# Optimization experiments

Measured on AMD Instinct MI355X. Metric: run time of the kernel, lower is better.

## Reference

```python
import jax, jax.numpy as jnp
import numpy as np

N, E, M, C = 4000, 60000, 16, 64        # nodes, edges, (lmax+1)^2, sphere_channels
H, HEADS, A, VC, CE, Z = 64, 8, 8, 8, 32, 90  # attn hidden, heads, alpha ch, value ch, edge ch, max elements


def _params(key):
    ks = jax.random.split(key, 10)
    g = lambda k, sh, fan: jax.random.normal(k, sh, dtype=jnp.float32) / np.float32(np.sqrt(fan))
    return [g(ks[0], (Z, CE), CE),          # emb_s: source atom embedding
            g(ks[1], (Z, CE), CE),          # emb_t: target atom embedding
            g(ks[2], (CE,), 1.0),           # w_d : distance projection
            g(ks[3], (CE, H), CE),          # We  : edge scalar -> hidden (m=0 inject)
            g(ks[4], (C, H), C),            # Ws  : source channel mix
            g(ks[5], (C, H), C),            # Wt  : target channel mix
            g(ks[6], (H, HEADS * A), H),    # Wa  : alpha features
            g(ks[7], (HEADS, A), A),        # va  : per-head alpha vector
            g(ks[8], (H, HEADS * VC), H),   # Wv  : values
            g(ks[9], (HEADS * VC, 1), HEADS * VC)]  # Wo : output proj (1 channel)


def setup_inputs() -> dict:
    key = jax.random.key(0)
    ks = jax.random.split(key, 8)
    x = jax.random.normal(ks[0], (N, M, C), dtype=jnp.float32)
    atomic_numbers = jax.random.randint(ks[1], (N,), 0, Z)
    edge_distance = jax.random.uniform(ks[2], (E,), dtype=jnp.float32) * 5.0 + 0.5
    edge_index = jax.random.randint(ks[3], (2, E), 0, N)
    noise_mask = jax.random.randint(ks[4], (N,), 0, 2).astype(bool)
    # per-edge SO3/Wigner rotation: random orthogonal [E, M, M]
    rng = np.random.default_rng(0)
    q, _ = np.linalg.qr(rng.standard_normal((E, M, M)).astype(np.float32))
    wigner = jnp.asarray(q, dtype=jnp.float32)
    names = ['emb_s', 'emb_t', 'w_d', 'We', 'Ws', 'Wt', 'Wa', 'va', 'Wv', 'Wo']
    inp = {'x': x, 'atomic_numbers': atomic_numbers, 'edge_distance': edge_distance,
           'edge_index': edge_index, 'noise_mask': noise_mask, 'wigner': wigner}
    for n, v in zip(names, _params(ks[5])):
        inp['fs_' + n] = v
    for n, v in zip(names, _params(ks[6])):
        inp['dn_' + n] = v
    return inp


def _block(x, zn, dist, src, dst, D, emb_s, emb_t, w_d, We, Ws, Wt, Wa, va, Wv, Wo):
    # gather + rotate edge-wise node features into edge-aligned frame
    xs = jnp.einsum('emn,enc->emc', D, x[src])            # [E,M,C]
    xt = jnp.einsum('emn,enc->emc', D, x[dst])            # [E,M,C]
    # scalar edge embedding (distance + source/target atom embeddings)
    e = jax.nn.silu(dist[:, None] * w_d + emb_s[zn[src]] + emb_t[zn[dst]])  # [E,CE]
    # SO2-style channel mixing; inject edge scalars into the m=0 (invariant) row
    f = jnp.einsum('emc,ch->emh', xs, Ws) + jnp.einsum('emc,ch->emh', xt, Wt)  # [E,M,H]
    f = f.at[:, 0, :].add(e @ We)
    # attention logits from the invariant part
    a = jax.nn.leaky_relu(f[:, 0, :] @ Wa, 0.2).reshape(E, HEADS, A)
    logits = jnp.einsum('eha,ha->eh', a, va)              # [E,HEADS]
    # segment softmax over incoming edges per target node
    mx = jax.ops.segment_max(logits, dst, num_segments=N)
    ex = jnp.exp(logits - mx[dst])
    alpha = ex / (jax.ops.segment_sum(ex, dst, num_segments=N)[dst] + 1e-9)
    # values, attention-weight, rotate back (D^T), scatter to nodes
    v = (f @ Wv).reshape(E, M, HEADS, VC) * alpha[:, None, :, None]
    v = jnp.einsum('emn,emhv->enhv', D, v).reshape(E, M, HEADS * VC)
    out = jax.ops.segment_sum(v, dst, num_segments=N) @ Wo  # [N,M,1]
    return out[:, 1:4, 0]  # narrow(1, 1, 3) -> l=1 vector components [N,3]


def reference(x, atomic_numbers, edge_distance, edge_index, noise_mask, wigner,
              fs_emb_s, fs_emb_t, fs_w_d, fs_We, fs_Ws, fs_Wt, fs_Wa, fs_va, fs_Wv, fs_Wo,
              dn_emb_s, dn_emb_t, dn_w_d, dn_We, dn_Ws, dn_Wt, dn_Wa, dn_va, dn_Wv, dn_Wo):
    src, dst = edge_index[0], edge_index[1]
    forces = _block(x, atomic_numbers, edge_distance, src, dst, wigner,
                    fs_emb_s, fs_emb_t, fs_w_d, fs_We, fs_Ws, fs_Wt, fs_Wa, fs_va, fs_Wv, fs_Wo)
    den = _block(x, atomic_numbers, edge_distance, src, dst, wigner,
                 dn_emb_s, dn_emb_t, dn_w_d, dn_We, dn_Ws, dn_Wt, dn_Wa, dn_va, dn_Wv, dn_Wo)
    # denoising_pos_forward with noise_mask: forces = den*mask + forces*~mask
    m = noise_mask[:, None].astype(x.dtype)
    return den * m + forces * (1.0 - m)
```

## Files before the change

kernel.cpp:

```cpp
#include <hip/hip_runtime.h>

typedef unsigned short ushort_t;
typedef __attribute__((ext_vector_type(8))) short short8;
typedef __attribute__((ext_vector_type(4))) float floatx4;

constexpr int RS = 11520;

__device__ inline float bf2f(ushort_t u) {
    union { unsigned int i; float f; } v; v.i = ((unsigned int)u) << 16; return v.f;
}
__device__ inline ushort_t f2bf(float f) {
    union { float f; unsigned int i; } v; v.f = f;
    unsigned int b = v.i + 0x7FFFu + ((v.i >> 16) & 1u);
    return (ushort_t)(b >> 16);
}

__global__ __launch_bounds__(256) void k_composites(
    const float* __restrict__ Ws0, const float* __restrict__ Wt0, const float* __restrict__ We0,
    const float* __restrict__ Wa0, const float* __restrict__ Wv0, const float* __restrict__ Wo0,
    const float* __restrict__ Ws1, const float* __restrict__ Wt1, const float* __restrict__ We1,
    const float* __restrict__ Wa1, const float* __restrict__ Wv1, const float* __restrict__ Wo1,
    float* __restrict__ cmp)
{
    int task = blockIdx.x;
    int r    = blockIdx.y;
    const float* Ws = r ? Ws1 : Ws0;
    const float* Wt = r ? Wt1 : Wt0;
    const float* We = r ? We1 : We0;
    const float* Wa = r ? Wa1 : Wa0;
    const float* Wv = r ? Wv1 : Wv0;
    const float* Wo = r ? Wo1 : Wo0;
    float* base = cmp + r * RS;

    if (task == 0 || task == 1) {
        const float* L = task ? Wt : Ws;
        float* out = base + task * 4096;
        for (int idx = threadIdx.x; idx < 4096; idx += 256) {
            int c = idx >> 6, j = idx & 63;
            float a = 0.f;
            for (int k = 0; k < 64; ++k) a += L[c * 64 + k] * Wa[k * 64 + j];
            out[idx] = a;
        }
    } else if (task == 2) {
        float* out = base + 8192;
        for (int idx = threadIdx.x; idx < 2048; idx += 256) {
            int ce = idx >> 6, j = idx & 63;
            float a = 0.f;
            for (int k = 0; k < 64; ++k) a += We[ce * 64 + k] * Wa[k * 64 + j];
            out[idx] = a;
        }
    } else {
        const float* L = (task == 3) ? Ws : (task == 4) ? Wt : We;
        int rows = (task == 5) ? 32 : 64;
        float* out = base + ((task == 3) ? 10240 : (task == 4) ? 10752 : 11264);
        for (int idx = threadIdx.x; idx < rows * 8; idx += 256) {
            int c = idx >> 3, h = idx & 7;
            float a = 0.f;
            for (int k = 0; k < 64; ++k) {
                float wv = 0.f;
                #pragma unroll
                for (int aa = 0; aa < 8; ++aa) wv += Wv[k * 64 + h * 8 + aa] * Wo[h * 8 + aa];
                a += L[c * 64 + k] * wv;
            }
            out[idx] = a;
        }
    }
}

__device__ inline short8 bfragW(const float* __restrict__ W, int colBase, int kBase,
                                int q, int n) {
    short8 f;
    #pragma unroll
    for (int j = 0; j < 8; ++j)
        f[j] = (short)f2bf(W[(kBase + q * 8 + j) * 64 + colBase + n]);
    return f;
}
__device__ inline short8 bfragP(const float* __restrict__ P0, const float* __restrict__ P1,
                                int kBase, int q, int n) {
    const float* P = (n < 8) ? P0 : P1;
    int c = n & 7;
    short8 f;
    #pragma unroll
    for (int j = 0; j < 8; ++j)
        f[j] = (short)f2bf(P[(kBase + q * 8 + j) * 8 + c]);
    return f;
}
__device__ inline void st4(ushort_t* dst, const floatx4& c) {
    uint2 v;
    v.x = (unsigned int)f2bf(c[0]) | ((unsigned int)f2bf(c[1]) << 16);
    v.y = (unsigned int)f2bf(c[2]) | ((unsigned int)f2bf(c[3]) << 16);
    *(uint2*)dst = v;
}

#define MFMA(a, b, c) __builtin_amdgcn_mfma_f32_16x16x32_bf16((a), (b), (c), 0, 0, 0)

__global__ __launch_bounds__(256, 2) void k_node(
    const float* __restrict__ x, const int* __restrict__ mask,
    const float* __restrict__ cmp,
    float* __restrict__ psrc, float* __restrict__ ptgt,
    ushort_t* __restrict__ srcA, ushort_t* __restrict__ tgtA,
    int N, int totWaves)
{
    int wid  = (int)((blockIdx.x * blockDim.x + threadIdx.x) >> 6);
    int lane = threadIdx.x & 63;
    int q    = lane >> 4;
    int n16  = lane & 15;

    short8 Bs0[4][2], Bs1[4][2], Bt0[4][2], Bt1[4][2];
    #pragma unroll
    for (int t = 0; t < 4; ++t) {
        #pragma unroll
        for (int kh = 0; kh < 2; ++kh) {
            Bs0[t][kh] = bfragW(cmp,             t * 16, kh * 32, q, n16);
            Bs1[t][kh] = bfragW(cmp + RS,        t * 16, kh * 32, q, n16);
            Bt0[t][kh] = bfragW(cmp + 4096,      t * 16, kh * 32, q, n16);
            Bt1[t][kh] = bfragW(cmp + RS + 4096, t * 16, kh * 32, q, n16);
        }
    }
    short8 Bp[2], Bq[2];
    #pragma unroll
    for (int kh = 0; kh < 2; ++kh) {
        Bp[kh] = bfragP(cmp + 10240, cmp + RS + 10240, kh * 32, q, n16);
        Bq[kh] = bfragP(cmp + 10752, cmp + RS + 10752, kh * 32, q, n16);
    }

    const floatx4 zero = {0.f, 0.f, 0.f, 0.f};

    for (int nd = wid; nd < N; nd += totWaves) {
        const float* xp = x + (size_t)nd * 1024 + n16 * 64 + q * 8;
        float4 v0 = *(const float4*)(xp);
        float4 v1 = *(const float4*)(xp + 4);
        float4 v2 = *(const float4*)(xp + 32);
        float4 v3 = *(const float4*)(xp + 36);
        short8 a0, a1;
        a0[0] = (short)f2bf(v0.x); a0[1] = (short)f2bf(v0.y);
        a0[2] = (short)f2bf(v0.z); a0[3] = (short)f2bf(v0.w);
        a0[4] = (short)f2bf(v1.x); a0[5] = (short)f2bf(v1.y);
        a0[6] = (short)f2bf(v1.z); a0[7] = (short)f2bf(v1.w);
        a1[0] = (short)f2bf(v2.x); a1[1] = (short)f2bf(v2.y);
        a1[2] = (short)f2bf(v2.z); a1[3] = (short)f2bf(v2.w);
        a1[4] = (short)f2bf(v3.x); a1[5] = (short)f2bf(v3.y);
        a1[6] = (short)f2bf(v3.z); a1[7] = (short)f2bf(v3.w);

        int rsel = (mask[nd] != 0);

        {
            floatx4 c0 = zero, c1 = zero, c2 = zero, c3 = zero;
            c0 = MFMA(a0, Bs0[0][0], c0); c0 = MFMA(a1, Bs0[0][1], c0);
            c1 = MFMA(a0, Bs0[1][0], c1); c1 = MFMA(a1, Bs0[1][1], c1);
            c2 = MFMA(a0, Bs0[2][0], c2); c2 = MFMA(a1, Bs0[2][1], c2);
            c3 = MFMA(a0, Bs0[3][0], c3); c3 = MFMA(a1, Bs0[3][1], c3);
            ushort_t* sp = srcA + (size_t)nd * 2048 + n16 * 16 + q * 4;
            st4(sp, c0); st4(sp + 256, c1); st4(sp + 512, c2); st4(sp + 768, c3);
        }
        {
            floatx4 c0 = zero, c1 = zero, c2 = zero, c3 = zero;
            c0 = MFMA(a0, Bs1[0][0], c0); c0 = MFMA(a1, Bs1[0][1], c0);
            c1 = MFMA(a0, Bs1[1][0], c1); c1 = MFMA(a1, Bs1[1][1], c1);
            c2 = MFMA(a0, Bs1[2][0], c2); c2 = MFMA(a1, Bs1[2][1], c2);
            c3 = MFMA(a0, Bs1[3][0], c3); c3 = MFMA(a1, Bs1[3][1], c3);
            ushort_t* sp = srcA + (size_t)nd * 2048 + 1024 + n16 * 16 + q * 4;
            st4(sp, c0); st4(sp + 256, c1); st4(sp + 512, c2); st4(sp + 768, c3);
        }

        {
            floatx4 c0 = zero, c1 = zero, c2 = zero, c3 = zero;
            if (rsel) {
                c0 = MFMA(a0, Bt1[0][0], c0); c0 = MFMA(a1, Bt1[0][1], c0);
                c1 = MFMA(a0, Bt1[1][0], c1); c1 = MFMA(a1, Bt1[1][1], c1);
                c2 = MFMA(a0, Bt1[2][0], c2); c2 = MFMA(a1, Bt1[2][1], c2);
                c3 = MFMA(a0, Bt1[3][0], c3); c3 = MFMA(a1, Bt1[3][1], c3);
            } else {
                c0 = MFMA(a0, Bt0[0][0], c0); c0 = MFMA(a1, Bt0[0][1], c0);
                c1 = MFMA(a0, Bt0[1][0], c1); c1 = MFMA(a1, Bt0[1][1], c1);
                c2 = MFMA(a0, Bt0[2][0], c2); c2 = MFMA(a1, Bt0[2][1], c2);
                c3 = MFMA(a0, Bt0[3][0], c3); c3 = MFMA(a1, Bt0[3][1], c3);
            }
            ushort_t* tp = tgtA + (size_t)nd * 1024 + n16 * 16 + q * 4;
            st4(tp, c0); st4(tp + 256, c1); st4(tp + 512, c2); st4(tp + 768, c3);
        }

        {
            floatx4 cp = zero;
            cp = MFMA(a0, Bp[0], cp); cp = MFMA(a1, Bp[1], cp);
            if (q == 0) {
                int r = n16 >> 3, h = n16 & 7;
                float* pp = psrc + (size_t)nd * 48 + r * 24 + h;
                pp[0]  = cp[1];
                pp[8]  = cp[2];
                pp[16] = cp[3];
            }
            floatx4 cq = zero;
            cq = MFMA(a0, Bq[0], cq); cq = MFMA(a1, Bq[1], cq);
            if (q == 0 && (n16 >> 3) == rsel) {
                int h = n16 & 7;
                float* pp = ptgt + (size_t)nd * 24 + h;
                pp[0]  = cq[1];
                pp[8]  = cq[2];
                pp[16] = cq[3];
            }
        }
    }
}

__global__ __launch_bounds__(256) void k_fused(
    const int* __restrict__ ei, const float* __restrict__ dist,
    const int* __restrict__ zn, const int* __restrict__ mask,
    const float* __restrict__ wig, const float* __restrict__ cmp,
    const float* __restrict__ embs0, const float* __restrict__ embt0, const float* __restrict__ wd0,
    const float* __restrict__ embs1, const float* __restrict__ embt1, const float* __restrict__ wd1,
    const float* __restrict__ va0, const float* __restrict__ va1,
    const ushort_t* __restrict__ srcA, const ushort_t* __restrict__ tgtA,
    const float* __restrict__ psrc, const float* __restrict__ ptgt,
    float* __restrict__ den, float* __restrict__ num, int E)
{
    int wv = threadIdx.x >> 6, j = threadIdx.x & 63;
    int e = blockIdx.x * 4 + wv;
    if (e >= E) return;
    int src = ei[e], dst = ei[E + e];
    int r = (mask[dst] != 0);
    float d = dist[e];
    int zs = zn[src], zt = zn[dst];
    int hq = j >> 3, h8 = j & 7;

    const float* w0 = wig + (size_t)e * 256;
    float4 wA = *(const float4*)(w0);
    float4 wB = *(const float4*)(w0 + 4);
    float4 wC = *(const float4*)(w0 + 8);
    float4 wD = *(const float4*)(w0 + 12);
    const ushort_t* sa = srcA + (size_t)src * 2048 + r * 1024 + j * 16;
    const ushort_t* ta = tgtA + (size_t)dst * 1024 + j * 16;
    short8 sv0 = *(const short8*)(sa);
    short8 sv1 = *(const short8*)(sa + 8);
    short8 tv0 = *(const short8*)(ta);
    short8 tv1 = *(const short8*)(ta + 8);
    float pv = 0.f;
    if (h8 < 3)
        pv = psrc[(size_t)src * 48 + r * 24 + h8 * 8 + hq]
           + ptgt[(size_t)dst * 24 + h8 * 8 + hq];

    float es;
    {
        int ce = j & 31;
        float z = r ? (d * wd1[ce] + embs1[zs * 32 + ce] + embt1[zt * 32 + ce])
                    : (d * wd0[ce] + embs0[zs * 32 + ce] + embt0[zt * 32 + ce]);
        es = z / (1.f + __expf(-z));
    }

    const float* WeWa   = cmp + r * RS + 8192;
    const float* WeWvWo = cmp + r * RS + 11264;
    float f0a = 0.f, ej = 0.f;
    #pragma unroll
    for (int ce = 0; ce < 32; ++ce) {
        float ev = __shfl(es, ce, 64);
        f0a += ev * WeWa[ce * 64 + j];
        ej  += ev * WeWvWo[ce * 8 + hq];
    }

    f0a += wA.x * (bf2f((ushort_t)sv0[0]) + bf2f((ushort_t)tv0[0]));
    f0a += wA.y * (bf2f((ushort_t)sv0[1]) + bf2f((ushort_t)tv0[1]));
    f0a += wA.z * (bf2f((ushort_t)sv0[2]) + bf2f((ushort_t)tv0[2]));
    f0a += wA.w * (bf2f((ushort_t)sv0[3]) + bf2f((ushort_t)tv0[3]));
    f0a += wB.x * (bf2f((ushort_t)sv0[4]) + bf2f((ushort_t)tv0[4]));
    f0a += wB.y * (bf2f((ushort_t)sv0[5]) + bf2f((ushort_t)tv0[5]));
    f0a += wB.z * (bf2f((ushort_t)sv0[6]) + bf2f((ushort_t)tv0[6]));
    f0a += wB.w * (bf2f((ushort_t)sv0[7]) + bf2f((ushort_t)tv0[7]));
    f0a += wC.x * (bf2f((ushort_t)sv1[0]) + bf2f((ushort_t)tv1[0]));
    f0a += wC.y * (bf2f((ushort_t)sv1[1]) + bf2f((ushort_t)tv1[1]));
    f0a += wC.z * (bf2f((ushort_t)sv1[2]) + bf2f((ushort_t)tv1[2]));
    f0a += wC.w * (bf2f((ushort_t)sv1[3]) + bf2f((ushort_t)tv1[3]));
    f0a += wD.x * (bf2f((ushort_t)sv1[4]) + bf2f((ushort_t)tv1[4]));
    f0a += wD.y * (bf2f((ushort_t)sv1[5]) + bf2f((ushort_t)tv1[5]));
    f0a += wD.z * (bf2f((ushort_t)sv1[6]) + bf2f((ushort_t)tv1[6]));
    f0a += wD.w * (bf2f((ushort_t)sv1[7]) + bf2f((ushort_t)tv1[7]));

    float la = f0a > 0.f ? f0a : 0.2f * f0a;
    float val = la * (r ? va1[j] : va0[j]);
    val += __shfl_xor(val, 1);
    val += __shfl_xor(val, 2);
    val += __shfl_xor(val, 4);
    float ex = __expf(val);

    if (h8 == 0) atomicAdd(&den[dst * 8 + hq], ex);
    if (h8 < 3) {
        float w0k = (h8 == 0) ? wA.y : (h8 == 1) ? wA.z : wA.w;
        atomicAdd(&num[dst * 24 + hq * 3 + h8], ex * (pv + ej * w0k));
    }
}

__global__ __launch_bounds__(256) void k_out(
    const float* __restrict__ num, const float* __restrict__ den,
    float* __restrict__ out, int N3)
{
    int t = blockIdx.x * 256 + threadIdx.x;
    if (t >= N3) return;
    int n = t / 3, k = t - n * 3;
    float acc = 0.f;
    #pragma unroll
    for (int h = 0; h < 8; ++h)
        acc += num[n * 24 + h * 3 + k] / (den[n * 8 + h] + 1e-9f);
    out[t] = acc;
}

extern "C" void kernel_launch(void* const* d_in, const int* in_sizes, int n_in,
                              void* d_out, int out_size, void* d_ws, size_t ws_size,
                              hipStream_t stream) {
    const float* x    = (const float*)d_in[0];
    const int*   zn   = (const int*)d_in[1];
    const float* dist = (const float*)d_in[2];
    const int*   ei   = (const int*)d_in[3];
    const int*   mask = (const int*)d_in[4];
    const float* wig  = (const float*)d_in[5];
    const float* fs[10]; const float* dn[10];
    for (int i = 0; i < 10; ++i) { fs[i] = (const float*)d_in[6 + i]; dn[i] = (const float*)d_in[16 + i]; }

    int N = in_sizes[1];
    int E = in_sizes[2];

    float* cmp  = (float*)d_ws;
    float* den  = cmp + 2 * RS;
    float* num  = den + (size_t)N * 8;
    float* psrc = num + (size_t)N * 24;
    float* ptgt = psrc + (size_t)N * 48;
    ushort_t* srcA = (ushort_t*)(ptgt + (size_t)N * 24);
    ushort_t* tgtA = srcA + (size_t)N * 2048;

    hipMemsetAsync(d_out, 0, (size_t)out_size * sizeof(float), stream);
    hipMemsetAsync(den, 0, (size_t)N * 32 * sizeof(float), stream);

    k_composites<<<dim3(6, 2), 256, 0, stream>>>(
        fs[4], fs[5], fs[3], fs[6], fs[8], fs[9],
        dn[4], dn[5], dn[3], dn[6], dn[8], dn[9], cmp);

    int nodeBlocks = 1000;
    int totWaves = nodeBlocks * (256 / 64);
    k_node<<<nodeBlocks, 256, 0, stream>>>(x, mask, cmp, psrc, ptgt, srcA, tgtA, N, totWaves);

    k_fused<<<(E + 3) / 4, 256, 0, stream>>>(
        ei, dist, zn, mask, wig, cmp,
        fs[0], fs[1], fs[2], dn[0], dn[1], dn[2],
        fs[7], dn[7], srcA, tgtA, psrc, ptgt, den, num, E);

    k_out<<<(N * 3 + 255) / 256, 256, 0, stream>>>(num, den, (float*)d_out, N * 3);
}
```

Before: 244.1 us.

## Prepack bf16 MFMA weight fragments, split composite kernel, process two edges per wave

The composite-weight kernel gains a z grid dimension that splits the Ws/Wt·Wa products across more blocks, and it writes those results directly as bf16 MFMA B-fragments into a packed buffer. k_node then loads each fragment with one short8 vector load instead of eight strided fp32 loads plus conversions per fragment in every wave. The fused edge kernel now handles two edges per wave, giving more independent loads in flight and halving the block count, at the cost of higher register pressure.

After: 246.5 us. Within noise of the previous version (+1.0%).

```diff
diff --git a/kernel.cpp b/kernel.cpp
--- a/kernel.cpp
+++ b/kernel.cpp
@@ -20,10 +20,11 @@
     const float* __restrict__ Wa0, const float* __restrict__ Wv0, const float* __restrict__ Wo0,
     const float* __restrict__ Ws1, const float* __restrict__ Wt1, const float* __restrict__ We1,
     const float* __restrict__ Wa1, const float* __restrict__ Wv1, const float* __restrict__ Wo1,
-    float* __restrict__ cmp)
+    float* __restrict__ cmp, ushort_t* __restrict__ packW)
 {
     int task = blockIdx.x;
     int r    = blockIdx.y;
+    int z    = blockIdx.z;
     const float* Ws = r ? Ws1 : Ws0;
     const float* Wt = r ? Wt1 : Wt0;
     const float* We = r ? We1 : We0;
@@ -34,22 +35,28 @@
 
     if (task == 0 || task == 1) {
         const float* L = task ? Wt : Ws;
-        float* out = base + task * 4096;
-        for (int idx = threadIdx.x; idx < 4096; idx += 256) {
-            int c = idx >> 6, j = idx & 63;
+        ushort_t* pw = packW + (r * 2 + task) * 4096;
+        int lo = z * 1024;
+        for (int idx = lo + threadIdx.x; idx < lo + 1024; idx += 256) {
+            int c = idx >> 6, jc = idx & 63;
             float a = 0.f;
-            for (int k = 0; k < 64; ++k) a += L[c * 64 + k] * Wa[k * 64 + j];
-            out[idx] = a;
+            #pragma unroll 8
+            for (int k = 0; k < 64; ++k) a += L[c * 64 + k] * Wa[k * 64 + jc];
+            int t = jc >> 4, n = jc & 15, kh = c >> 5, q = (c >> 3) & 3, jj = c & 7;
+            pw[((t * 2 + kh) * 64 + q * 16 + n) * 8 + jj] = f2bf(a);
         }
     } else if (task == 2) {
         float* out = base + 8192;
-        for (int idx = threadIdx.x; idx < 2048; idx += 256) {
-            int ce = idx >> 6, j = idx & 63;
+        int lo = z * 512;
+        for (int idx = lo + threadIdx.x; idx < lo + 512; idx += 256) {
+            int ce = idx >> 6, jc = idx & 63;
             float a = 0.f;
-            for (int k = 0; k < 64; ++k) a += We[ce * 64 + k] * Wa[k * 64 + j];
+            #pragma unroll 8
+            for (int k = 0; k < 64; ++k) a += We[ce * 64 + k] * Wa[k * 64 + jc];
             out[idx] = a;
         }
     } else {
+        if (z != 0) return;
         const float* L = (task == 3) ? Ws : (task == 4) ? Wt : We;
         int rows = (task == 5) ? 32 : 64;
         float* out = base + ((task == 3) ? 10240 : (task == 4) ? 10752 : 11264);
@@ -67,14 +74,6 @@
     }
 }
 
-__device__ inline short8 bfragW(const float* __restrict__ W, int colBase, int kBase,
-                                int q, int n) {
-    short8 f;
-    #pragma unroll
-    for (int j = 0; j < 8; ++j)
-        f[j] = (short)f2bf(W[(kBase + q * 8 + j) * 64 + colBase + n]);
-    return f;
-}
 __device__ inline short8 bfragP(const float* __restrict__ P0, const float* __restrict__ P1,
                                 int kBase, int q, int n) {
     const float* P = (n < 8) ? P0 : P1;
@@ -96,7 +95,7 @@
 
 __global__ __launch_bounds__(256, 2) void k_node(
     const float* __restrict__ x, const int* __restrict__ mask,
-    const float* __restrict__ cmp,
+    const float* __restrict__ cmp, const ushort_t* __restrict__ packW,
     float* __restrict__ psrc, float* __restrict__ ptgt,
     ushort_t* __restrict__ srcA, ushort_t* __restrict__ tgtA,
     int N, int totWaves)
@@ -111,10 +110,11 @@
     for (int t = 0; t < 4; ++t) {
         #pragma unroll
         for (int kh = 0; kh < 2; ++kh) {
-            Bs0[t][kh] = bfragW(cmp,             t * 16, kh * 32, q, n16);
-            Bs1[t][kh] = bfragW(cmp + RS,        t * 16, kh * 32, q, n16);
-            Bt0[t][kh] = bfragW(cmp + 4096,      t * 16, kh * 32, q, n16);
-            Bt1[t][kh] = bfragW(cmp + RS + 4096, t * 16, kh * 32, q, n16);
+            int fo = (t * 2 + kh) * 512 + lane * 8;
+            Bs0[t][kh] = *(const short8*)(packW +           fo);
+            Bt0[t][kh] = *(const short8*)(packW +  4096 +   fo);
+            Bs1[t][kh] = *(const short8*)(packW +  8192 +   fo);
+            Bt1[t][kh] = *(const short8*)(packW + 12288 +   fo);
         }
     }
     short8 Bp[2], Bq[2];
@@ -215,76 +215,108 @@
     float* __restrict__ den, float* __restrict__ num, int E)
 {
     int wv = threadIdx.x >> 6, j = threadIdx.x & 63;
-    int e = blockIdx.x * 4 + wv;
-    if (e >= E) return;
-    int src = ei[e], dst = ei[E + e];
-    int r = (mask[dst] != 0);
-    float d = dist[e];
-    int zs = zn[src], zt = zn[dst];
+    int e0 = blockIdx.x * 8 + wv * 2;
+    if (e0 >= E) return;
+    int e1 = e0 + 1;
+    bool has1 = (e1 < E);
+    int e1c = has1 ? e1 : e0;
+
     int hq = j >> 3, h8 = j & 7;
 
-    const float* w0 = wig + (size_t)e * 256;
-    float4 wA = *(const float4*)(w0);
-    float4 wB = *(const float4*)(w0 + 4);
-    float4 wC = *(const float4*)(w0 + 8);
-    float4 wD = *(const float4*)(w0 + 12);
-    const ushort_t* sa = srcA + (size_t)src * 2048 + r * 1024 + j * 16;
-    const ushort_t* ta = tgtA + (size_t)dst * 1024 + j * 16;
-    short8 sv0 = *(const short8*)(sa);
-    short8 sv1 = *(const short8*)(sa + 8);
-    short8 tv0 = *(const short8*)(ta);
-    short8 tv1 = *(const short8*)(ta + 8);
-    float pv = 0.f;
-    if (h8 < 3)
-        pv = psrc[(size_t)src * 48 + r * 24 + h8 * 8 + hq]
-           + ptgt[(size_t)dst * 24 + h8 * 8 + hq];
-
-    float es;
+    int src0 = ei[e0], dst0 = ei[E + e0];
+    int src1 = ei[e1c], dst1 = ei[E + e1c];
+    int r0 = (mask[dst0] != 0), r1 = (mask[dst1] != 0);
+    float d0 = dist[e0], d1 = dist[e1c];
+    int zs0 = zn[src0], zt0 = zn[dst0];
+    int zs1 = zn[src1], zt1 = zn[dst1];
+
+    const float* w0p = wig + (size_t)e0 * 256;
+    const float* w1p = wig + (size_t)e1c * 256;
+    float4 wA0 = *(const float4*)(w0p),     wA1 = *(const float4*)(w1p);
+    float4 wB0 = *(const float4*)(w0p + 4), wB1 = *(const float4*)(w1p + 4);
+    float4 wC0 = *(const float4*)(w0p + 8), wC1 = *(const float4*)(w1p + 8);
+    float4 wD0 = *(const float4*)(w0p + 12),wD1 = *(const float4*)(w1p + 12);
+    const ushort_t* sa0 = srcA + (size_t)src0 * 2048 + r0 * 1024 + j * 16;
+    const ushort_t* ta0 = tgtA + (size_t)dst0 * 1024 + j * 16;
+    const ushort_t* sa1 = srcA + (size_t)src1 * 2048 + r1 * 1024 + j * 16;
+    const ushort_t* ta1 = tgtA + (size_t)dst1 * 1024 + j * 16;
+    short8 sv00 = *(const short8*)(sa0),     sv01 = *(const short8*)(sa0 + 8);
+    short8 tv00 = *(const short8*)(ta0),     tv01 = *(const short8*)(ta0 + 8);
+    short8 sv10 = *(const short8*)(sa1),     sv11 = *(const short8*)(sa1 + 8);
+    short8 tv10 = *(const short8*)(ta1),     tv11 = *(const short8*)(ta1 + 8);
+    float pv0 = 0.f, pv1 = 0.f;
+    if (h8 < 3) {
+        pv0 = psrc[(size_t)src0 * 48 + r0 * 24 + h8 * 8 + hq]
+            + ptgt[(size_t)dst0 * 24 + h8 * 8 + hq];
+        pv1 = psrc[(size_t)src1 * 48 + r1 * 24 + h8 * 8 + hq]
+            + ptgt[(size_t)dst1 * 24 + h8 * 8 + hq];
+    }
+
+    float es0, es1;
     {
         int ce = j & 31;
-        float z = r ? (d * wd1[ce] + embs1[zs * 32 + ce] + embt1[zt * 32 + ce])
-                    : (d * wd0[ce] + embs0[zs * 32 + ce] + embt0[zt * 32 + ce]);
-        es = z / (1.f + __expf(-z));
-    }
-
-    const float* WeWa   = cmp + r * RS + 8192;
-    const float* WeWvWo = cmp + r * RS + 11264;
-    float f0a = 0.f, ej = 0.f;
+        float z0 = r0 ? (d0 * wd1[ce] + embs1[zs0 * 32 + ce] + embt1[zt0 * 32 + ce])
+                      : (d0 * wd0[ce] + embs0[zs0 * 32 + ce] + embt0[zt0 * 32 + ce]);
+        float z1 = r1 ? (d1 * wd1[ce] + embs1[zs1 * 32 + ce] + embt1[zt1 * 32 + ce])
+                      : (d1 * wd0[ce] + embs0[zs1 * 32 + ce] + embt0[zt1 * 32 + ce]);
+        es0 = z0 / (1.f + __expf(-z0));
+        es1 = z1 / (1.f + __expf(-z1));
+    }
+
+    const float* WeWa_0   = cmp + r0 * RS + 8192;
+    const float* WeWvWo_0 = cmp + r0 * RS + 11264;
+    const float* WeWa_1   = cmp + r1 * RS + 8192;
+    const float* WeWvWo_1 = cmp + r1 * RS + 11264;
+    float f0a0 = 0.f, ej0 = 0.f, f0a1 = 0.f, ej1 = 0.f;
     #pragma unroll
     for (int ce = 0; ce < 32; ++ce) {
-        float ev = __shfl(es, ce, 64);
-        f0a += ev * WeWa[ce * 64 + j];
-        ej  += ev * WeWvWo[ce * 8 + hq];
-    }
-
-    f0a += wA.x * (bf2f((ushort_t)sv0[0]) + bf2f((ushort_t)tv0[0]));
-    f0a += wA.y * (bf2f((ushort_t)sv0[1]) + bf2f((ushort_t)tv0[1]));
-    f0a += wA.z * (bf2f((ushort_t)sv0[2]) + bf2f((ushort_t)tv0[2]));
-    f0a += wA.w * (bf2f((ushort_t)sv0[3]) + bf2f((ushort_t)tv0[3]));
-    f0a += wB.x * (bf2f((ushort_t)sv0[4]) + bf2f((ushort_t)tv0[4]));
-    f0a += wB.y * (bf2f((ushort_t)sv0[5]) + bf2f((ushort_t)tv0[5]));
-    f0a += wB.z * (bf2f((ushort_t)sv0[6]) + bf2f((ushort_t)tv0[6]));
-    f0a += wB.w * (bf2f((ushort_t)sv0[7]) + bf2f((ushort_t)tv0[7]));
-    f0a += wC.x * (bf2f((ushort_t)sv1[0]) + bf2f((ushort_t)tv1[0]));
-    f0a += wC.y * (bf2f((ushort_t)sv1[1]) + bf2f((ushort_t)tv1[1]));
-    f0a += wC.z * (bf2f((ushort_t)sv1[2]) + bf2f((ushort_t)tv1[2]));
-    f0a += wC.w * (bf2f((ushort_t)sv1[3]) + bf2f((ushort_t)tv1[3]));
-    f0a += wD.x * (bf2f((ushort_t)sv1[4]) + bf2f((ushort_t)tv1[4]));
-    f0a += wD.y * (bf2f((ushort_t)sv1[5]) + bf2f((ushort_t)tv1[5]));
-    f0a += wD.z * (bf2f((ushort_t)sv1[6]) + bf2f((ushort_t)tv1[6]));
-    f0a += wD.w * (bf2f((ushort_t)sv1[7]) + bf2f((ushort_t)tv1[7]));
-
-    float la = f0a > 0.f ? f0a : 0.2f * f0a;
-    float val = la * (r ? va1[j] : va0[j]);
-    val += __shfl_xor(val, 1);
-    val += __shfl_xor(val, 2);
-    val += __shfl_xor(val, 4);
-    float ex = __expf(val);
-
-    if (h8 == 0) atomicAdd(&den[dst * 8 + hq], ex);
+        float ev0 = __shfl(es0, ce, 64);
+        float ev1 = __shfl(es1, ce, 64);
+        f0a0 += ev0 * WeWa_0[ce * 64 + j];
+        f0a1 += ev1 * WeWa_1[ce * 64 + j];
+        ej0  += ev0 * WeWvWo_0[ce * 8 + hq];
+        ej1  += ev1 * WeWvWo_1[ce * 8 + hq];
+    }
+
+    #define ACC(F, W, SV, TV, i0) \
+        F += W * (bf2f((ushort_t)SV[i0]) + bf2f((ushort_t)TV[i0]));
+    ACC(f0a0, wA0.x, sv00, tv00, 0) ACC(f0a0, wA0.y, sv00, tv00, 1)
+    ACC(f0a0, wA0.z, sv00, tv00, 2) ACC(f0a0, wA0.w, sv00, tv00, 3)
+    ACC(f0a0, wB0.x, sv00, tv00, 4) ACC(f0a0, wB0.y, sv00, tv00, 5)
+    ACC(f0a0, wB0.z, sv00, tv00, 6) ACC(f0a0, wB0.w, sv00, tv00, 7)
+    ACC(f0a0, wC0.x, sv01, tv01, 0) ACC(f0a0, wC0.y, sv01, tv01, 1)
+    ACC(f0a0, wC0.z, sv01, tv01, 2) ACC(f0a0, wC0.w, sv01, tv01, 3)
+    ACC(f0a0, wD0.x, sv01, tv01, 4) ACC(f0a0, wD0.y, sv01, tv01, 5)
+    ACC(f0a0, wD0.z, sv01, tv01, 6) ACC(f0a0, wD0.w, sv01, tv01, 7)
+    ACC(f0a1, wA1.x, sv10, tv10, 0) ACC(f0a1, wA1.y, sv10, tv10, 1)
+    ACC(f0a1, wA1.z, sv10, tv10, 2) ACC(f0a1, wA1.w, sv10, tv10, 3)
+    ACC(f0a1, wB1.x, sv10, tv10, 4) ACC(f0a1, wB1.y, sv10, tv10, 5)
+    ACC(f0a1, wB1.z, sv10, tv10, 6) ACC(f0a1, wB1.w, sv10, tv10, 7)
+    ACC(f0a1, wC1.x, sv11, tv11, 0) ACC(f0a1, wC1.y, sv11, tv11, 1)
+    ACC(f0a1, wC1.z, sv11, tv11, 2) ACC(f0a1, wC1.w, sv11, tv11, 3)
+    ACC(f0a1, wD1.x, sv11, tv11, 4) ACC(f0a1, wD1.y, sv11, tv11, 5)
+    ACC(f0a1, wD1.z, sv11, tv11, 6) ACC(f0a1, wD1.w, sv11, tv11, 7)
+    #undef ACC
+
+    float la0 = f0a0 > 0.f ? f0a0 : 0.2f * f0a0;
+    float la1 = f0a1 > 0.f ? f0a1 : 0.2f * f0a1;
+    float val0 = la0 * (r0 ? va1[j] : va0[j]);
+    float val1 = la1 * (r1 ? va1[j] : va0[j]);
+    val0 += __shfl_xor(val0, 1); val1 += __shfl_xor(val1, 1);
+    val0 += __shfl_xor(val0, 2); val1 += __shfl_xor(val1, 2);
+    val0 += __shfl_xor(val0, 4); val1 += __shfl_xor(val1, 4);
+    float ex0 = __expf(val0);
+    float ex1 = __expf(val1);
+
+    if (h8 == 0) {
+        atomicAdd(&den[dst0 * 8 + hq], ex0);
+        if (has1) atomicAdd(&den[dst1 * 8 + hq], ex1);
+    }
     if (h8 < 3) {
-        float w0k = (h8 == 0) ? wA.y : (h8 == 1) ? wA.z : wA.w;
-        atomicAdd(&num[dst * 24 + hq * 3 + h8], ex * (pv + ej * w0k));
+        float w0k0 = (h8 == 0) ? wA0.y : (h8 == 1) ? wA0.z : wA0.w;
+        float w0k1 = (h8 == 0) ? wA1.y : (h8 == 1) ? wA1.z : wA1.w;
+        atomicAdd(&num[dst0 * 24 + hq * 3 + h8], ex0 * (pv0 + ej0 * w0k0));
+        if (has1) atomicAdd(&num[dst1 * 24 + hq * 3 + h8], ex1 * (pv1 + ej1 * w0k1));
     }
 }
 
@@ -324,19 +356,20 @@
     float* ptgt = psrc + (size_t)N * 48;
     ushort_t* srcA = (ushort_t*)(ptgt + (size_t)N * 24);
     ushort_t* tgtA = srcA + (size_t)N * 2048;
+    ushort_t* packW = tgtA + (size_t)N * 1024;
 
     hipMemsetAsync(d_out, 0, (size_t)out_size * sizeof(float), stream);
     hipMemsetAsync(den, 0, (size_t)N * 32 * sizeof(float), stream);
 
-    k_composites<<<dim3(6, 2), 256, 0, stream>>>(
+    k_composites<<<dim3(6, 2, 4), 256, 0, stream>>>(
         fs[4], fs[5], fs[3], fs[6], fs[8], fs[9],
-        dn[4], dn[5], dn[3], dn[6], dn[8], dn[9], cmp);
+        dn[4], dn[5], dn[3], dn[6], dn[8], dn[9], cmp, packW);
 
     int nodeBlocks = 1000;
     int totWaves = nodeBlocks * (256 / 64);
-    k_node<<<nodeBlocks, 256, 0, stream>>>(x, mask, cmp, psrc, ptgt, srcA, tgtA, N, totWaves);
-
-    k_fused<<<(E + 3) / 4, 256, 0, stream>>>(
+    k_node<<<nodeBlocks, 256, 0, stream>>>(x, mask, cmp, packW, psrc, ptgt, srcA, tgtA, N, totWaves);
+
+    k_fused<<<(E + 7) / 8, 256, 0, stream>>>(
         ei, dist, zn, mask, wig, cmp,
         fs[0], fs[1], fs[2], dn[0], dn[1], dn[2],
         fs[7], dn[7], srcA, tgtA, psrc, ptgt, den, num, E);
```

## Prepack bf16 MFMA weight fragments, split composite kernel, fold memsets into node kernel

Applied to the files above, without the earlier changes.

k_composites now writes the Ws·Wa and Wt·Wa composites straight into a bf16 layout matching the MFMA B fragments, so each k_node wave loads them with one short8 vector load instead of converting 64 strided floats. The composite grid gains a z dimension to spread that work over more blocks. The two hipMemsetAsync calls are removed, and k_node zeroes the den/num accumulators itself. The d_out memset is dropped, which relies on k_out writing every output element.

Result: faster. 225.1 us (-7.8%).

```diff
diff --git a/kernel.cpp b/kernel.cpp
--- a/kernel.cpp
+++ b/kernel.cpp
@@ -20,10 +20,11 @@
     const float* __restrict__ Wa0, const float* __restrict__ Wv0, const float* __restrict__ Wo0,
     const float* __restrict__ Ws1, const float* __restrict__ Wt1, const float* __restrict__ We1,
     const float* __restrict__ Wa1, const float* __restrict__ Wv1, const float* __restrict__ Wo1,
-    float* __restrict__ cmp)
+    float* __restrict__ cmp, ushort_t* __restrict__ packW)
 {
     int task = blockIdx.x;
     int r    = blockIdx.y;
+    int z    = blockIdx.z;
     const float* Ws = r ? Ws1 : Ws0;
     const float* Wt = r ? Wt1 : Wt0;
     const float* We = r ? We1 : We0;
@@ -34,22 +35,28 @@
 
     if (task == 0 || task == 1) {
         const float* L = task ? Wt : Ws;
-        float* out = base + task * 4096;
-        for (int idx = threadIdx.x; idx < 4096; idx += 256) {
-            int c = idx >> 6, j = idx & 63;
+        ushort_t* pw = packW + (r * 2 + task) * 4096;
+        int lo = z * 1024;
+        for (int idx = lo + threadIdx.x; idx < lo + 1024; idx += 256) {
+            int c = idx >> 6, jc = idx & 63;
             float a = 0.f;
-            for (int k = 0; k < 64; ++k) a += L[c * 64 + k] * Wa[k * 64 + j];
-            out[idx] = a;
+            #pragma unroll 8
+            for (int k = 0; k < 64; ++k) a += L[c * 64 + k] * Wa[k * 64 + jc];
+            int t = jc >> 4, n = jc & 15, kh = c >> 5, q = (c >> 3) & 3, jj = c & 7;
+            pw[((t * 2 + kh) * 64 + q * 16 + n) * 8 + jj] = f2bf(a);
         }
     } else if (task == 2) {
         float* out = base + 8192;
-        for (int idx = threadIdx.x; idx < 2048; idx += 256) {
-            int ce = idx >> 6, j = idx & 63;
+        int lo = z * 512;
+        for (int idx = lo + threadIdx.x; idx < lo + 512; idx += 256) {
+            int ce = idx >> 6, jc = idx & 63;
             float a = 0.f;
-            for (int k = 0; k < 64; ++k) a += We[ce * 64 + k] * Wa[k * 64 + j];
+            #pragma unroll 8
+            for (int k = 0; k < 64; ++k) a += We[ce * 64 + k] * Wa[k * 64 + jc];
             out[idx] = a;
         }
     } else {
+        if (z != 0) return;
         const float* L = (task == 3) ? Ws : (task == 4) ? Wt : We;
         int rows = (task == 5) ? 32 : 64;
         float* out = base + ((task == 3) ? 10240 : (task == 4) ? 10752 : 11264);
@@ -67,14 +74,6 @@
     }
 }
 
-__device__ inline short8 bfragW(const float* __restrict__ W, int colBase, int kBase,
-                                int q, int n) {
-    short8 f;
-    #pragma unroll
-    for (int j = 0; j < 8; ++j)
-        f[j] = (short)f2bf(W[(kBase + q * 8 + j) * 64 + colBase + n]);
-    return f;
-}
 __device__ inline short8 bfragP(const float* __restrict__ P0, const float* __restrict__ P1,
                                 int kBase, int q, int n) {
     const float* P = (n < 8) ? P0 : P1;
@@ -96,9 +95,10 @@
 
 __global__ __launch_bounds__(256, 2) void k_node(
     const float* __restrict__ x, const int* __restrict__ mask,
-    const float* __restrict__ cmp,
+    const float* __restrict__ cmp, const ushort_t* __restrict__ packW,
     float* __restrict__ psrc, float* __restrict__ ptgt,
     ushort_t* __restrict__ srcA, ushort_t* __restrict__ tgtA,
+    float* __restrict__ den, float* __restrict__ num,
     int N, int totWaves)
 {
     int wid  = (int)((blockIdx.x * blockDim.x + threadIdx.x) >> 6);
@@ -111,10 +111,11 @@
     for (int t = 0; t < 4; ++t) {
         #pragma unroll
         for (int kh = 0; kh < 2; ++kh) {
-            Bs0[t][kh] = bfragW(cmp,             t * 16, kh * 32, q, n16);
-            Bs1[t][kh] = bfragW(cmp + RS,        t * 16, kh * 32, q, n16);
-            Bt0[t][kh] = bfragW(cmp + 4096,      t * 16, kh * 32, q, n16);
-            Bt1[t][kh] = bfragW(cmp + RS + 4096, t * 16, kh * 32, q, n16);
+            int fo = (t * 2 + kh) * 512 + lane * 8;
+            Bs0[t][kh] = *(const short8*)(packW +           fo);
+            Bt0[t][kh] = *(const short8*)(packW +  4096 +   fo);
+            Bs1[t][kh] = *(const short8*)(packW +  8192 +   fo);
+            Bt1[t][kh] = *(const short8*)(packW + 12288 +   fo);
         }
     }
     short8 Bp[2], Bq[2];
@@ -127,6 +128,9 @@
     const floatx4 zero = {0.f, 0.f, 0.f, 0.f};
 
     for (int nd = wid; nd < N; nd += totWaves) {
+        if (lane < 8)  den[nd * 8 + lane] = 0.f;
+        if (lane < 24) num[nd * 24 + lane] = 0.f;
+
         const float* xp = x + (size_t)nd * 1024 + n16 * 64 + q * 8;
         float4 v0 = *(const float4*)(xp);
         float4 v1 = *(const float4*)(xp + 4);
@@ -324,17 +328,17 @@
     float* ptgt = psrc + (size_t)N * 48;
     ushort_t* srcA = (ushort_t*)(ptgt + (size_t)N * 24);
     ushort_t* tgtA = srcA + (size_t)N * 2048;
-
-    hipMemsetAsync(d_out, 0, (size_t)out_size * sizeof(float), stream);
-    hipMemsetAsync(den, 0, (size_t)N * 32 * sizeof(float), stream);
-
-    k_composites<<<dim3(6, 2), 256, 0, stream>>>(
+    ushort_t* packW = tgtA + (size_t)N * 1024;
+
+
+    k_composites<<<dim3(6, 2, 4), 256, 0, stream>>>(
         fs[4], fs[5], fs[3], fs[6], fs[8], fs[9],
-        dn[4], dn[5], dn[3], dn[6], dn[8], dn[9], cmp);
+        dn[4], dn[5], dn[3], dn[6], dn[8], dn[9], cmp, packW);
 
     int nodeBlocks = 1000;
     int totWaves = nodeBlocks * (256 / 64);
-    k_node<<<nodeBlocks, 256, 0, stream>>>(x, mask, cmp, psrc, ptgt, srcA, tgtA, N, totWaves);
+    k_node<<<nodeBlocks, 256, 0, stream>>>(x, mask, cmp, packW, psrc, ptgt,
+                                           srcA, tgtA, den, num, N, totWaves);
 
     k_fused<<<(E + 3) / 4, 256, 0, stream>>>(
         ei, dist, zn, mask, wig, cmp,
```
